# Kernel optimization log

Measured on AMD Instinct MI355X. Metric: run time of the kernel, lower is better.

The kernel has to match this reference:

```python
import jax, jax.numpy as jnp
import numpy as np

N = 50000      # total nodes in batch
E = 640000     # directed edges
G = 64         # graphs in batch
F_IN = 24      # node features
H = 128        # hidden dim
L = 4          # num GCN layers
BN_EPS = 1e-5


def setup_inputs() -> dict:
    key = jax.random.key(0)
    ks = jax.random.split(key, 12)
    s = 0.05  # weight init scale
    return {
        "x": jax.random.normal(ks[0], (N, F_IN), jnp.float32),
        "edge_index": jax.random.randint(ks[1], (2, E), 0, N, dtype=jnp.int32),
        "batch": jnp.sort(jax.random.randint(ks[2], (N,), 0, G, dtype=jnp.int32)),
        "W0": jax.random.normal(ks[3], (F_IN, H), jnp.float32) * s,
        "Wh": jax.random.normal(ks[4], (L - 1, H, H), jnp.float32) * s,
        "b": jnp.zeros((L, H), jnp.float32),
        "bn_gamma": jnp.ones((L, H), jnp.float32),
        "bn_beta": jnp.zeros((L, H), jnp.float32),
        "bn_mean": jax.random.normal(ks[5], (L, H), jnp.float32) * 0.01,
        "bn_var": jnp.ones((L, H), jnp.float32),
        "pool_W": jax.random.normal(ks[6], (2 * H, H), jnp.float32) * s,
        "pool_b": jnp.zeros((H,), jnp.float32),
        "out_W": jax.random.normal(ks[7], (H, H // 2), jnp.float32) * s,
        "out_b": jnp.zeros((H // 2,), jnp.float32),
    }


def reference(x, edge_index, batch, W0, Wh, b, bn_gamma, bn_beta, bn_mean,
              bn_var, pool_W, pool_b, out_W, out_b):
    n = x.shape[0]
    loop = jnp.arange(n, dtype=edge_index.dtype)
    src = jnp.concatenate([edge_index[0], loop])  # [E+N] with self-loops
    dst = jnp.concatenate([edge_index[1], loop])
    # symmetric GCN normalization: deg includes self-loops, so deg >= 1
    deg = jax.ops.segment_sum(jnp.ones_like(dst, x.dtype), dst, num_segments=n)
    dis = jax.lax.rsqrt(deg)
    coef = (dis[src] * dis[dst])[:, None]  # [E+N, 1]

    def gcn_conv(h, W, bias):
        h = h @ W                                   # [N, H]
        msg = h[src] * coef                         # gather + scale
        return jax.ops.segment_sum(msg, dst, num_segments=n) + bias

    Ws = [W0] + [Wh[i] for i in range(Wh.shape[0])]
    h = x
    for i in range(L):
        h = gcn_conv(h, Ws[i], b[i])
        # BatchNorm1d (eval mode) + ReLU; dropout = identity in eval
        h = (h - bn_mean[i]) * jax.lax.rsqrt(bn_var[i] + BN_EPS) * bn_gamma[i] + bn_beta[i]
        h = jax.nn.relu(h)

    counts = jax.ops.segment_sum(jnp.ones((n,), h.dtype), batch, num_segments=G)
    x_mean = jax.ops.segment_sum(h, batch, num_segments=G) / jnp.maximum(counts, 1.0)[:, None]
    x_max = jax.ops.segment_max(h, batch, num_segments=G)
    x_pooled = jnp.concatenate([x_mean, x_max], axis=1)        # [G, 2H]
    x_pooled = jax.nn.relu(x_pooled @ pool_W + pool_b)         # global_pool MLP
    return x_pooled @ out_W + out_b                            # embedding head [G, H//2]
```

## Files before the change

kernel.cpp:

```cpp
#include <hip/hip_runtime.h>
#include <hip/hip_bf16.h>
#include <hip/hip_fp16.h>

#define HD 128
#define BN_EPS 1e-5f
#define PSPLIT 16

typedef __attribute__((ext_vector_type(8))) short short8;
typedef __attribute__((ext_vector_type(4))) float f32x4;

__device__ inline unsigned short f2bf(float v, float& rem) {
    unsigned u = __float_as_uint(v);
    unsigned r = (u + 0x7FFFu + ((u >> 16) & 1u)) >> 16;
    rem = v - __uint_as_float(r << 16);
    return (unsigned short)r;
}

__global__ void k_count(const int* __restrict__ dst, int* __restrict__ counts, int E) {
    int i = blockIdx.x * blockDim.x + threadIdx.x;
    for (; i < E; i += gridDim.x * blockDim.x)
        atomicAdd(&counts[dst[i]], 1);
}

__global__ void k_scan1(const int* __restrict__ counts, int* __restrict__ offs,
                        int* __restrict__ bsums, int n) {
    __shared__ int s[256];
    int t = threadIdx.x, i = blockIdx.x * 256 + t;
    int v = (i < n) ? counts[i] : 0;
    s[t] = v; __syncthreads();
    for (int d = 1; d < 256; d <<= 1) {
        int x = (t >= d) ? s[t - d] : 0;
        __syncthreads(); s[t] += x; __syncthreads();
    }
    if (i < n) offs[i] = s[t] - v;
    if (t == 255) bsums[blockIdx.x] = s[255];
}

__global__ void k_scan2(int* __restrict__ bsums, int nb) {
    __shared__ int s[256];
    int t = threadIdx.x;
    int v = (t < nb) ? bsums[t] : 0;
    s[t] = v; __syncthreads();
    for (int d = 1; d < 256; d <<= 1) {
        int x = (t >= d) ? s[t - d] : 0;
        __syncthreads(); s[t] += x; __syncthreads();
    }
    if (t < nb) bsums[t] = s[t] - v;
}

__global__ void k_scan3(int* __restrict__ offs, const int* __restrict__ bsums,
                        int* __restrict__ cursor, const int* __restrict__ counts,
                        float* __restrict__ dis, int n) {
    int i = blockIdx.x * 256 + threadIdx.x;
    if (i < n) {
        int v = offs[i] + bsums[blockIdx.x];
        offs[i] = v;
        cursor[i] = v;
        dis[i] = rsqrtf((float)(counts[i] + 1));
    }
}

__global__ void k_fill(const int* __restrict__ src, const int* __restrict__ dst,
                       int* __restrict__ cursor, unsigned short* __restrict__ esrc, int E) {
    int i = blockIdx.x * blockDim.x + threadIdx.x;
    for (; i < E; i += gridDim.x * blockDim.x) {
        int s = src[i], d = dst[i];
        int pos = atomicAdd(&cursor[d], 1);
        esrc[pos] = (unsigned short)s;
    }
}

__global__ void k_wsplit(const float* __restrict__ W0, const float* __restrict__ Wh,
                         unsigned short* __restrict__ whi, unsigned short* __restrict__ wlo) {
    int idx = blockIdx.x * 256 + threadIdx.x;
    int l = idx >> 14, rest = idx & 16383;
    int k = rest >> 7, c = rest & 127;
    float val;
    if (l == 0) {
        if (k >= 32) return;
        val = (k < 24) ? W0[k * HD + c] : 0.f;
    } else {
        val = Wh[(size_t)(l - 1) * HD * HD + (size_t)k * HD + c];
    }
    float rem, rem2;
    unsigned short hi = f2bf(val, rem);
    unsigned short lo = f2bf(rem, rem2);
    int cb = c >> 4, kc = k >> 5;
    int lane = (c & 15) | (((k & 31) >> 3) << 4);
    int j = k & 7;
    size_t addr;
    if (l == 0) addr = (size_t)(cb * 64 + lane) * 8 + j;
    else        addr = (size_t)l * 16384 + (size_t)((cb * 4 + kc) * 64 + lane) * 8 + j;
    whi[addr] = hi; wlo[addr] = lo;
}

__global__ void k_agg_x(const float* __restrict__ in, const int* __restrict__ offs,
                        const int* __restrict__ counts, const unsigned short* __restrict__ esrc,
                        const float* __restrict__ dis, unsigned short* __restrict__ ohi,
                        unsigned short* __restrict__ olo, int n) {
    const int FQ = 6, GRP = 8;
    int grp = threadIdx.x / GRP;
    int lane = threadIdx.x % GRP;
    int node = blockIdx.x * (blockDim.x / GRP) + grp;
    if (node >= n) return;
    int rowblk = node >> 4, rr = node & 15;

    if (lane == FQ) {
        size_t base = (size_t)rowblk * 512 + (size_t)(rr + 48) * 8;
        ushort4 z = make_ushort4(0, 0, 0, 0);
        *(ushort4*)(ohi + base) = z; *(ushort4*)(ohi + base + 4) = z;
        *(ushort4*)(olo + base) = z; *(ushort4*)(olo + base + 4) = z;
    }
    if (lane >= FQ) return;

    const float4* in4 = reinterpret_cast<const float4*>(in);
    float dn = dis[node];
    float sl = dn * dn;
    float4 a = in4[(size_t)node * FQ + lane];
    float4 accA = make_float4(sl * a.x, sl * a.y, sl * a.z, sl * a.w);
    float4 accB = make_float4(0.f, 0.f, 0.f, 0.f);

    int e = offs[node], end = e + counts[node];
    for (; e + 3 < end; e += 4) {
        int s0 = esrc[e],     s1 = esrc[e + 1];
        int s2 = esrc[e + 2], s3 = esrc[e + 3];
        float c0 = dis[s0] * dn, c1 = dis[s1] * dn;
        float c2 = dis[s2] * dn, c3 = dis[s3] * dn;
        float4 v0 = in4[(size_t)s0 * FQ + lane];
        float4 v1 = in4[(size_t)s1 * FQ + lane];
        float4 v2 = in4[(size_t)s2 * FQ + lane];
        float4 v3 = in4[(size_t)s3 * FQ + lane];
        accA.x = fmaf(c0, v0.x, fmaf(c2, v2.x, accA.x));
        accA.y = fmaf(c0, v0.y, fmaf(c2, v2.y, accA.y));
        accA.z = fmaf(c0, v0.z, fmaf(c2, v2.z, accA.z));
        accA.w = fmaf(c0, v0.w, fmaf(c2, v2.w, accA.w));
        accB.x = fmaf(c1, v1.x, fmaf(c3, v3.x, accB.x));
        accB.y = fmaf(c1, v1.y, fmaf(c3, v3.y, accB.y));
        accB.z = fmaf(c1, v1.z, fmaf(c3, v3.z, accB.z));
        accB.w = fmaf(c1, v1.w, fmaf(c3, v3.w, accB.w));
    }
    for (; e < end; ++e) {
        int s0 = esrc[e];
        float c0 = dis[s0] * dn;
        float4 v0 = in4[(size_t)s0 * FQ + lane];
        accA.x = fmaf(c0, v0.x, accA.x);
        accA.y = fmaf(c0, v0.y, accA.y);
        accA.z = fmaf(c0, v0.z, accA.z);
        accA.w = fmaf(c0, v0.w, accA.w);
    }
    float4 acc = make_float4(accA.x + accB.x, accA.y + accB.y,
                             accA.z + accB.z, accA.w + accB.w);

    int f0 = lane * 4;
    int lidx = rr | (((f0 & 31) >> 3) << 4);
    int j0 = f0 & 7;
    size_t base = (size_t)rowblk * 512 + (size_t)lidx * 8 + j0;
    float r0, r1, r2, r3, d0;
    ushort4 hi, lo;
    hi.x = f2bf(acc.x, r0); hi.y = f2bf(acc.y, r1);
    hi.z = f2bf(acc.z, r2); hi.w = f2bf(acc.w, r3);
    lo.x = f2bf(r0, d0); lo.y = f2bf(r1, d0);
    lo.z = f2bf(r2, d0); lo.w = f2bf(r3, d0);
    *(ushort4*)(ohi + base) = hi;
    *(ushort4*)(olo + base) = lo;
}

__global__ void k_agg_h(const __half* __restrict__ in, const int* __restrict__ offs,
                        const int* __restrict__ counts, const unsigned short* __restrict__ esrc,
                        const float* __restrict__ dis, unsigned short* __restrict__ ohi,
                        unsigned short* __restrict__ olo, int n) {
    int grp = threadIdx.x >> 5;
    int lane = threadIdx.x & 31;
    int node = blockIdx.x * 8 + grp;
    if (node >= n) return;
    int rowblk = node >> 4, rr = node & 15;

    const float2* in8 = reinterpret_cast<const float2*>(in);
    float dn = dis[node];
    float sl = dn * dn;

    float2 raw = in8[(size_t)node * 32 + lane];
    __half2 p0 = *(__half2*)&raw.x, p1 = *(__half2*)&raw.y;
    float2 f0v = __half22float2(p0), f1v = __half22float2(p1);
    float4 accA = make_float4(sl * f0v.x, sl * f0v.y, sl * f1v.x, sl * f1v.y);
    float4 accB = make_float4(0.f, 0.f, 0.f, 0.f);

    int e = offs[node], end = e + counts[node];
    for (; e + 3 < end; e += 4) {
        int s0 = esrc[e],     s1 = esrc[e + 1];
        int s2 = esrc[e + 2], s3 = esrc[e + 3];
        float c0 = dis[s0] * dn, c1 = dis[s1] * dn;
        float c2 = dis[s2] * dn, c3 = dis[s3] * dn;
        float2 w0 = in8[(size_t)s0 * 32 + lane];
        float2 w1 = in8[(size_t)s1 * 32 + lane];
        float2 w2 = in8[(size_t)s2 * 32 + lane];
        float2 w3 = in8[(size_t)s3 * 32 + lane];
        float2 a0 = __half22float2(*(__half2*)&w0.x), b0 = __half22float2(*(__half2*)&w0.y);
        float2 a1 = __half22float2(*(__half2*)&w1.x), b1 = __half22float2(*(__half2*)&w1.y);
        float2 a2 = __half22float2(*(__half2*)&w2.x), b2 = __half22float2(*(__half2*)&w2.y);
        float2 a3 = __half22float2(*(__half2*)&w3.x), b3 = __half22float2(*(__half2*)&w3.y);
        accA.x = fmaf(c0, a0.x, fmaf(c2, a2.x, accA.x));
        accA.y = fmaf(c0, a0.y, fmaf(c2, a2.y, accA.y));
        accA.z = fmaf(c0, b0.x, fmaf(c2, b2.x, accA.z));
        accA.w = fmaf(c0, b0.y, fmaf(c2, b2.y, accA.w));
        accB.x = fmaf(c1, a1.x, fmaf(c3, a3.x, accB.x));
        accB.y = fmaf(c1, a1.y, fmaf(c3, a3.y, accB.y));
        accB.z = fmaf(c1, b1.x, fmaf(c3, b3.x, accB.z));
        accB.w = fmaf(c1, b1.y, fmaf(c3, b3.y, accB.w));
    }
    for (; e < end; ++e) {
        int s0 = esrc[e];
        float c0 = dis[s0] * dn;
        float2 w0 = in8[(size_t)s0 * 32 + lane];
        float2 a0 = __half22float2(*(__half2*)&w0.x), b0 = __half22float2(*(__half2*)&w0.y);
        accA.x = fmaf(c0, a0.x, accA.x);
        accA.y = fmaf(c0, a0.y, accA.y);
        accA.z = fmaf(c0, b0.x, accA.z);
        accA.w = fmaf(c0, b0.y, accA.w);
    }
    float4 acc = make_float4(accA.x + accB.x, accA.y + accB.y,
                             accA.z + accB.z, accA.w + accB.w);

    int f0 = lane * 4;
    int kc = f0 >> 5;
    int lidx = rr | (((f0 & 31) >> 3) << 4);
    int j0 = f0 & 7;
    size_t base = ((size_t)rowblk * 4 + kc) * 512 + (size_t)lidx * 8 + j0;
    float r0, r1, r2, r3, d0;
    ushort4 hi, lo;
    hi.x = f2bf(acc.x, r0); hi.y = f2bf(acc.y, r1);
    hi.z = f2bf(acc.z, r2); hi.w = f2bf(acc.w, r3);
    lo.x = f2bf(r0, d0); lo.y = f2bf(r1, d0);
    lo.z = f2bf(r2, d0); lo.w = f2bf(r3, d0);
    *(ushort4*)(ohi + base) = hi;
    *(ushort4*)(olo + base) = lo;
}

template<int KC, bool OUT_F16>
__global__ __launch_bounds__(256) void k_gemm_m(
        const unsigned short* __restrict__ agh, const unsigned short* __restrict__ agl,
        const unsigned short* __restrict__ wh, const unsigned short* __restrict__ wl,
        const float* __restrict__ bias, const float* __restrict__ gamma,
        const float* __restrict__ beta, const float* __restrict__ mean,
        const float* __restrict__ var, float* __restrict__ outf,
        __half* __restrict__ outh, int n) {
    __shared__ unsigned short lbh[8 * KC * 512];
    __shared__ unsigned short lbl[8 * KC * 512];
    int tid = threadIdx.x;
    for (int i = tid; i < 1024 * KC; i += 256) {
        ((ushort4*)lbh)[i] = ((const ushort4*)wh)[i];
        ((ushort4*)lbl)[i] = ((const ushort4*)wl)[i];
    }
    __syncthreads();

    int wave = tid >> 6, lane = tid & 63;
    int grb0 = blockIdx.x * 8 + wave * 2;

    f32x4 acc[2][8] = {};

    for (int kc = 0; kc < KC; ++kc) {
        short8 a0h = *(const short8*)(agh + ((size_t)grb0 * KC + kc) * 512 + lane * 8);
        short8 a0l = *(const short8*)(agl + ((size_t)grb0 * KC + kc) * 512 + lane * 8);
        short8 a1h = *(const short8*)(agh + ((size_t)(grb0 + 1) * KC + kc) * 512 + lane * 8);
        short8 a1l = *(const short8*)(agl + ((size_t)(grb0 + 1) * KC + kc) * 512 + lane * 8);
        #pragma unroll
        for (int cb = 0; cb < 8; ++cb) {
            short8 bh = *(const short8*)(lbh + (size_t)((cb * KC + kc) * 64 + lane) * 8);
            short8 bl = *(const short8*)(lbl + (size_t)((cb * KC + kc) * 64 + lane) * 8);
            acc[0][cb] = __builtin_amdgcn_mfma_f32_16x16x32_bf16(a0h, bh, acc[0][cb], 0, 0, 0);
            acc[0][cb] = __builtin_amdgcn_mfma_f32_16x16x32_bf16(a0h, bl, acc[0][cb], 0, 0, 0);
            acc[0][cb] = __builtin_amdgcn_mfma_f32_16x16x32_bf16(a0l, bh, acc[0][cb], 0, 0, 0);
            acc[1][cb] = __builtin_amdgcn_mfma_f32_16x16x32_bf16(a1h, bh, acc[1][cb], 0, 0, 0);
            acc[1][cb] = __builtin_amdgcn_mfma_f32_16x16x32_bf16(a1h, bl, acc[1][cb], 0, 0, 0);
            acc[1][cb] = __builtin_amdgcn_mfma_f32_16x16x32_bf16(a1l, bh, acc[1][cb], 0, 0, 0);
        }
    }

    int colbase = lane & 15;
    float scv[8], shv[8];
    #pragma unroll
    for (int cb = 0; cb < 8; ++cb) {
        int c = cb * 16 + colbase;
        float s = gamma[c] * rsqrtf(var[c] + BN_EPS);
        scv[cb] = s;
        shv[cb] = beta[c] + (bias[c] - mean[c]) * s;
    }
    int r0 = (lane >> 4) * 4;
    #pragma unroll
    for (int rb = 0; rb < 2; ++rb) {
        int rowb = (grb0 + rb) * 16 + r0;
        #pragma unroll
        for (int rg = 0; rg < 4; ++rg) {
            int row = rowb + rg;
            if (row < n) {
                #pragma unroll
                for (int cb = 0; cb < 8; ++cb) {
                    float v = fmaxf(fmaf(acc[rb][cb][rg], scv[cb], shv[cb]), 0.f);
                    if (OUT_F16)
                        outh[(size_t)row * HD + cb * 16 + colbase] = __float2half(v);
                    else
                        outf[(size_t)row * HD + cb * 16 + colbase] = v;
                }
            }
        }
    }
}

__global__ void k_bounds(const int* __restrict__ batch, int* __restrict__ starts,
                         int n, int G) {
    int g = threadIdx.x;
    if (g > G) return;
    int lo = 0, hi = n;
    while (lo < hi) {
        int mid = (lo + hi) >> 1;
        if (batch[mid] < g) lo = mid + 1; else hi = mid;
    }
    starts[g] = lo;
}

__global__ void k_pool(const float* __restrict__ h, const int* __restrict__ starts,
                       float* __restrict__ gsum, unsigned int* __restrict__ gmax) {
    int g = blockIdx.x;
    int slice = blockIdx.y;
    int t = threadIdx.x;
    int s = starts[g], e = starts[g + 1];
    int cnt = e - s;
    int per = (cnt + PSPLIT - 1) / PSPLIT;
    int beg = s + slice * per;
    int end = min(beg + per, e);
    if (beg >= end) return;
    float sum = 0.f, mx = 0.f;
    for (int node = beg; node < end; ++node) {
        float v = h[(size_t)node * HD + t];
        sum += v;
        mx = fmaxf(mx, v);
    }
    atomicAdd(&gsum[g * HD + t], sum);
    atomicMax(&gmax[g * HD + t], __float_as_uint(mx));
}

__global__ void k_mlp1(const float* __restrict__ gsum, const unsigned int* __restrict__ gmax,
                       const int* __restrict__ starts, const float* __restrict__ pool_W,
                       const float* __restrict__ pool_b, float* __restrict__ hid) {
    int g = blockIdx.x, t = threadIdx.x;
    __shared__ float pooled[2 * HD];
    float cntf = fmaxf((float)(starts[g + 1] - starts[g]), 1.f);
    pooled[t] = gsum[g * HD + t] / cntf;
    pooled[HD + t] = __uint_as_float(gmax[g * HD + t]);
    __syncthreads();
    float acc = pool_b[t];
    for (int k = 0; k < 2 * HD; ++k)
        acc += pooled[k] * pool_W[k * HD + t];
    hid[g * HD + t] = fmaxf(acc, 0.f);
}

__global__ void k_mlp2(const float* __restrict__ hid, const float* __restrict__ out_W,
                       const float* __restrict__ out_b, float* __restrict__ out) {
    int g = blockIdx.x, o = threadIdx.x;
    __shared__ float hv[HD];
    hv[o] = hid[g * HD + o];
    hv[o + 64] = hid[g * HD + o + 64];
    __syncthreads();
    float acc = out_b[o];
    for (int j = 0; j < HD; ++j)
        acc += hv[j] * out_W[j * 64 + o];
    out[g * 64 + o] = acc;
}

extern "C" void kernel_launch(void* const* d_in, const int* in_sizes, int n_in,
                              void* d_out, int out_size, void* d_ws, size_t ws_size,
                              hipStream_t stream) {
    const float* x        = (const float*)d_in[0];
    const int*   eidx     = (const int*)d_in[1];
    const int*   batch    = (const int*)d_in[2];
    const float* W0       = (const float*)d_in[3];
    const float* Wh       = (const float*)d_in[4];
    const float* b        = (const float*)d_in[5];
    const float* bn_gamma = (const float*)d_in[6];
    const float* bn_beta  = (const float*)d_in[7];
    const float* bn_mean  = (const float*)d_in[8];
    const float* bn_var   = (const float*)d_in[9];
    const float* pool_W   = (const float*)d_in[10];
    const float* pool_b   = (const float*)d_in[11];
    const float* out_W    = (const float*)d_in[12];
    const float* out_b    = (const float*)d_in[13];
    float* out = (float*)d_out;

    const int N = in_sizes[2];
    const int E = in_sizes[1] / 2;
    const int L = in_sizes[5] / HD;
    const int G = out_size / (HD / 2);

    const int* src = eidx;
    const int* dst = eidx + E;

    const int NBLK = (N + 127) / 128;
    const size_t NRB = (size_t)NBLK * 8;

    char* p = (char*)d_ws;
    float*  h    = (float*)p;  p += (size_t)N * HD * 4;
    __half* hf   = (__half*)p; p += (size_t)NBLK * 128 * HD * 2;
    unsigned short* agh = (unsigned short*)p; p += NRB * 4 * 512 * 2;
    unsigned short* agl = (unsigned short*)p; p += NRB * 4 * 512 * 2;
    unsigned short* whi = (unsigned short*)p; p += (size_t)4 * 16384 * 2;
    unsigned short* wlo = (unsigned short*)p; p += (size_t)4 * 16384 * 2;
    unsigned short* esrc = (unsigned short*)p; p += (((size_t)E * 2 + 15) & ~15ull);
    int*   counts  = (int*)p;   p += (size_t)N * 4;
    float* dis     = (float*)p; p += (size_t)N * 4;
    int*   offs    = (int*)p;   p += (size_t)(N + 1) * 4;
    int*   cursor  = (int*)p;   p += (size_t)N * 4;
    int*   bsums   = (int*)p;   p += 256 * 4;
    float* gsum    = (float*)p; p += (size_t)G * HD * 4;
    unsigned int* gmax = (unsigned int*)p; p += (size_t)G * HD * 4;
    int*   starts  = (int*)p;   p += (size_t)(G + 1) * 4;
    float* hid     = (float*)p; p += (size_t)G * HD * 4;
    (void)ws_size; (void)n_in;

    hipMemsetAsync(counts, 0, (size_t)N * 4, stream);
    hipMemsetAsync(gsum, 0, (size_t)G * HD * 8, stream);

    const int NB = (N + 255) / 256;

    k_count<<<1024, 256, 0, stream>>>(dst, counts, E);
    k_scan1<<<NB, 256, 0, stream>>>(counts, offs, bsums, N);
    k_scan2<<<1, 256, 0, stream>>>(bsums, NB);
    k_scan3<<<NB, 256, 0, stream>>>(offs, bsums, cursor, counts, dis, N);
    k_fill<<<1024, 256, 0, stream>>>(src, dst, cursor, esrc, E);
    k_bounds<<<1, 128, 0, stream>>>(batch, starts, N, G);
    k_wsplit<<<256, 256, 0, stream>>>(W0, Wh, whi, wlo);

    k_agg_x<<<(N + 31) / 32, 256, 0, stream>>>(x, offs, counts, esrc, dis, agh, agl, N);
    k_gemm_m<1, true><<<NBLK, 256, 0, stream>>>(agh, agl, whi, wlo, b, bn_gamma, bn_beta,
                                                bn_mean, bn_var, nullptr, hf, N);

    for (int l = 1; l < L; ++l) {
        k_agg_h<<<(N + 7) / 8, 256, 0, stream>>>(hf, offs, counts, esrc, dis, agh, agl, N);
        if (l < L - 1)
            k_gemm_m<4, true><<<NBLK, 256, 0, stream>>>(agh, agl,
                whi + (size_t)l * 16384, wlo + (size_t)l * 16384,
                b + l * HD, bn_gamma + l * HD, bn_beta + l * HD,
                bn_mean + l * HD, bn_var + l * HD, nullptr, hf, N);
        else
            k_gemm_m<4, false><<<NBLK, 256, 0, stream>>>(agh, agl,
                whi + (size_t)l * 16384, wlo + (size_t)l * 16384,
                b + l * HD, bn_gamma + l * HD, bn_beta + l * HD,
                bn_mean + l * HD, bn_var + l * HD, h, nullptr, N);
    }

    dim3 pgrid(G, PSPLIT);
    k_pool<<<pgrid, HD, 0, stream>>>(h, starts, gsum, gmax);
    k_mlp1<<<G, HD, 0, stream>>>(gsum, gmax, starts, pool_W, pool_b, hid);
    k_mlp2<<<G, 64, 0, stream>>>(hid, out_W, out_b, out);
}
```

Measured before the change: 281.9 us.

## Use single fp16 activations with split fp16 weights for hidden GCN layers

Hidden-layer aggregation now writes one fp16 copy of the aggregated features instead of a bf16 hi/lo pair. The hidden GEMM uses fp16 MFMA with only two products per tile (activation times weight hi and lo) instead of three bf16 products. This halves the aggregation write and GEMM read traffic and cuts MFMA work, at the cost of lower activation precision from fp16 rounding. Separately, the batch-bounds kernel is folded into scan2 and the two head MLP kernels are merged into one, removing launches.

```diff
diff --git a/kernel.cpp b/kernel.cpp
--- a/kernel.cpp
+++ b/kernel.cpp
@@ -7,6 +7,7 @@
 #define PSPLIT 16
 
 typedef __attribute__((ext_vector_type(8))) short short8;
+typedef __attribute__((ext_vector_type(8))) _Float16 half8;
 typedef __attribute__((ext_vector_type(4))) float f32x4;
 
 __device__ inline unsigned short f2bf(float v, float& rem) {
@@ -36,7 +37,9 @@
     if (t == 255) bsums[blockIdx.x] = s[255];
 }
 
-__global__ void k_scan2(int* __restrict__ bsums, int nb) {
+__global__ void k_scan2(int* __restrict__ bsums, int nb,
+                        const int* __restrict__ batch, int* __restrict__ starts,
+                        int n, int G) {
     __shared__ int s[256];
     int t = threadIdx.x;
     int v = (t < nb) ? bsums[t] : 0;
@@ -46,6 +49,14 @@
         __syncthreads(); s[t] += x; __syncthreads();
     }
     if (t < nb) bsums[t] = s[t] - v;
+    if (t <= G) {
+        int lo = 0, hi = n;
+        while (lo < hi) {
+            int mid = (lo + hi) >> 1;
+            if (batch[mid] < t) lo = mid + 1; else hi = mid;
+        }
+        starts[t] = lo;
+    }
 }
 
 __global__ void k_scan3(int* __restrict__ offs, const int* __restrict__ bsums,
@@ -71,27 +82,31 @@
 }
 
 __global__ void k_wsplit(const float* __restrict__ W0, const float* __restrict__ Wh,
-                         unsigned short* __restrict__ whi, unsigned short* __restrict__ wlo) {
+                         unsigned short* __restrict__ whi0, unsigned short* __restrict__ wlo0,
+                         unsigned short* __restrict__ whf, unsigned short* __restrict__ wlf) {
     int idx = blockIdx.x * 256 + threadIdx.x;
     int l = idx >> 14, rest = idx & 16383;
     int k = rest >> 7, c = rest & 127;
-    float val;
-    if (l == 0) {
-        if (k >= 32) return;
-        val = (k < 24) ? W0[k * HD + c] : 0.f;
-    } else {
-        val = Wh[(size_t)(l - 1) * HD * HD + (size_t)k * HD + c];
-    }
-    float rem, rem2;
-    unsigned short hi = f2bf(val, rem);
-    unsigned short lo = f2bf(rem, rem2);
     int cb = c >> 4, kc = k >> 5;
     int lane = (c & 15) | (((k & 31) >> 3) << 4);
     int j = k & 7;
-    size_t addr;
-    if (l == 0) addr = (size_t)(cb * 64 + lane) * 8 + j;
-    else        addr = (size_t)l * 16384 + (size_t)((cb * 4 + kc) * 64 + lane) * 8 + j;
-    whi[addr] = hi; wlo[addr] = lo;
+    if (l == 0) {
+        if (k >= 32) return;
+        float val = (k < 24) ? W0[k * HD + c] : 0.f;
+        float rem, rem2;
+        unsigned short hi = f2bf(val, rem);
+        unsigned short lo = f2bf(rem, rem2);
+        size_t addr = (size_t)(cb * 64 + lane) * 8 + j;
+        whi0[addr] = hi; wlo0[addr] = lo;
+    } else {
+        float val = Wh[(size_t)(l - 1) * HD * HD + (size_t)k * HD + c];
+        __half h = __float2half(val);
+        float rem = val - __half2float(h);
+        __half lo = __float2half(rem);
+        size_t addr = (size_t)(l - 1) * 16384 + (size_t)((cb * 4 + kc) * 64 + lane) * 8 + j;
+        whf[addr] = __half_as_ushort(h);
+        wlf[addr] = __half_as_ushort(lo);
+    }
 }
 
 __global__ void k_agg_x(const float* __restrict__ in, const int* __restrict__ offs,
@@ -167,8 +182,7 @@
 
 __global__ void k_agg_h(const __half* __restrict__ in, const int* __restrict__ offs,
                         const int* __restrict__ counts, const unsigned short* __restrict__ esrc,
-                        const float* __restrict__ dis, unsigned short* __restrict__ ohi,
-                        unsigned short* __restrict__ olo, int n) {
+                        const float* __restrict__ dis, unsigned short* __restrict__ af, int n) {
     int grp = threadIdx.x >> 5;
     int lane = threadIdx.x & 31;
     int node = blockIdx.x * 8 + grp;
@@ -226,28 +240,89 @@
     int lidx = rr | (((f0 & 31) >> 3) << 4);
     int j0 = f0 & 7;
     size_t base = ((size_t)rowblk * 4 + kc) * 512 + (size_t)lidx * 8 + j0;
-    float r0, r1, r2, r3, d0;
-    ushort4 hi, lo;
-    hi.x = f2bf(acc.x, r0); hi.y = f2bf(acc.y, r1);
-    hi.z = f2bf(acc.z, r2); hi.w = f2bf(acc.w, r3);
-    lo.x = f2bf(r0, d0); lo.y = f2bf(r1, d0);
-    lo.z = f2bf(r2, d0); lo.w = f2bf(r3, d0);
-    *(ushort4*)(ohi + base) = hi;
-    *(ushort4*)(olo + base) = lo;
-}
-
-template<int KC, bool OUT_F16>
+    ushort4 hv;
+    hv.x = __half_as_ushort(__float2half(acc.x));
+    hv.y = __half_as_ushort(__float2half(acc.y));
+    hv.z = __half_as_ushort(__float2half(acc.z));
+    hv.w = __half_as_ushort(__float2half(acc.w));
+    *(ushort4*)(af + base) = hv;
+}
+
 __global__ __launch_bounds__(256) void k_gemm_m(
         const unsigned short* __restrict__ agh, const unsigned short* __restrict__ agl,
         const unsigned short* __restrict__ wh, const unsigned short* __restrict__ wl,
         const float* __restrict__ bias, const float* __restrict__ gamma,
         const float* __restrict__ beta, const float* __restrict__ mean,
+        const float* __restrict__ var, __half* __restrict__ outh, int n) {
+    __shared__ unsigned short lbh[8 * 512];
+    __shared__ unsigned short lbl[8 * 512];
+    int tid = threadIdx.x;
+    for (int i = tid; i < 1024; i += 256) {
+        ((ushort4*)lbh)[i] = ((const ushort4*)wh)[i];
+        ((ushort4*)lbl)[i] = ((const ushort4*)wl)[i];
+    }
+    __syncthreads();
+
+    int wave = tid >> 6, lane = tid & 63;
+    int grb0 = blockIdx.x * 8 + wave * 2;
+
+    f32x4 acc[2][8] = {};
+
+    short8 a0h = *(const short8*)(agh + (size_t)grb0 * 512 + lane * 8);
+    short8 a0l = *(const short8*)(agl + (size_t)grb0 * 512 + lane * 8);
+    short8 a1h = *(const short8*)(agh + (size_t)(grb0 + 1) * 512 + lane * 8);
+    short8 a1l = *(const short8*)(agl + (size_t)(grb0 + 1) * 512 + lane * 8);
+    #pragma unroll
+    for (int cb = 0; cb < 8; ++cb) {
+        short8 bh = *(const short8*)(lbh + (size_t)(cb * 64 + lane) * 8);
+        short8 bl = *(const short8*)(lbl + (size_t)(cb * 64 + lane) * 8);
+        acc[0][cb] = __builtin_amdgcn_mfma_f32_16x16x32_bf16(a0h, bh, acc[0][cb], 0, 0, 0);
+        acc[0][cb] = __builtin_amdgcn_mfma_f32_16x16x32_bf16(a0h, bl, acc[0][cb], 0, 0, 0);
+        acc[0][cb] = __builtin_amdgcn_mfma_f32_16x16x32_bf16(a0l, bh, acc[0][cb], 0, 0, 0);
+        acc[1][cb] = __builtin_amdgcn_mfma_f32_16x16x32_bf16(a1h, bh, acc[1][cb], 0, 0, 0);
+        acc[1][cb] = __builtin_amdgcn_mfma_f32_16x16x32_bf16(a1h, bl, acc[1][cb], 0, 0, 0);
+        acc[1][cb] = __builtin_amdgcn_mfma_f32_16x16x32_bf16(a1l, bh, acc[1][cb], 0, 0, 0);
+    }
+
+    int colbase = lane & 15;
+    float scv[8], shv[8];
+    #pragma unroll
+    for (int cb = 0; cb < 8; ++cb) {
+        int c = cb * 16 + colbase;
+        float s = gamma[c] * rsqrtf(var[c] + BN_EPS);
+        scv[cb] = s;
+        shv[cb] = beta[c] + (bias[c] - mean[c]) * s;
+    }
+    int r0 = (lane >> 4) * 4;
+    #pragma unroll
+    for (int rb = 0; rb < 2; ++rb) {
+        int rowb = (grb0 + rb) * 16 + r0;
+        #pragma unroll
+        for (int rg = 0; rg < 4; ++rg) {
+            int row = rowb + rg;
+            if (row < n) {
+                #pragma unroll
+                for (int cb = 0; cb < 8; ++cb) {
+                    float v = fmaxf(fmaf(acc[rb][cb][rg], scv[cb], shv[cb]), 0.f);
+                    outh[(size_t)row * HD + cb * 16 + colbase] = __float2half(v);
+                }
+            }
+        }
+    }
+}
+
+template<bool OUT_F16>
+__global__ __launch_bounds__(256) void k_gemm_h(
+        const unsigned short* __restrict__ af,
+        const unsigned short* __restrict__ wh, const unsigned short* __restrict__ wl,
+        const float* __restrict__ bias, const float* __restrict__ gamma,
+        const float* __restrict__ beta, const float* __restrict__ mean,
         const float* __restrict__ var, float* __restrict__ outf,
         __half* __restrict__ outh, int n) {
-    __shared__ unsigned short lbh[8 * KC * 512];
-    __shared__ unsigned short lbl[8 * KC * 512];
+    __shared__ unsigned short lbh[16384];
+    __shared__ unsigned short lbl[16384];
     int tid = threadIdx.x;
-    for (int i = tid; i < 1024 * KC; i += 256) {
+    for (int i = tid; i < 4096; i += 256) {
         ((ushort4*)lbh)[i] = ((const ushort4*)wh)[i];
         ((ushort4*)lbl)[i] = ((const ushort4*)wl)[i];
     }
@@ -258,21 +333,18 @@
 
     f32x4 acc[2][8] = {};
 
-    for (int kc = 0; kc < KC; ++kc) {
-        short8 a0h = *(const short8*)(agh + ((size_t)grb0 * KC + kc) * 512 + lane * 8);
-        short8 a0l = *(const short8*)(agl + ((size_t)grb0 * KC + kc) * 512 + lane * 8);
-        short8 a1h = *(const short8*)(agh + ((size_t)(grb0 + 1) * KC + kc) * 512 + lane * 8);
-        short8 a1l = *(const short8*)(agl + ((size_t)(grb0 + 1) * KC + kc) * 512 + lane * 8);
+    #pragma unroll
+    for (int kc = 0; kc < 4; ++kc) {
+        half8 a0 = *(const half8*)(af + ((size_t)grb0 * 4 + kc) * 512 + lane * 8);
+        half8 a1 = *(const half8*)(af + ((size_t)(grb0 + 1) * 4 + kc) * 512 + lane * 8);
         #pragma unroll
         for (int cb = 0; cb < 8; ++cb) {
-            short8 bh = *(const short8*)(lbh + (size_t)((cb * KC + kc) * 64 + lane) * 8);
-            short8 bl = *(const short8*)(lbl + (size_t)((cb * KC + kc) * 64 + lane) * 8);
-            acc[0][cb] = __builtin_amdgcn_mfma_f32_16x16x32_bf16(a0h, bh, acc[0][cb], 0, 0, 0);
-            acc[0][cb] = __builtin_amdgcn_mfma_f32_16x16x32_bf16(a0h, bl, acc[0][cb], 0, 0, 0);
-            acc[0][cb] = __builtin_amdgcn_mfma_f32_16x16x32_bf16(a0l, bh, acc[0][cb], 0, 0, 0);
-            acc[1][cb] = __builtin_amdgcn_mfma_f32_16x16x32_bf16(a1h, bh, acc[1][cb], 0, 0, 0);
-            acc[1][cb] = __builtin_amdgcn_mfma_f32_16x16x32_bf16(a1h, bl, acc[1][cb], 0, 0, 0);
-            acc[1][cb] = __builtin_amdgcn_mfma_f32_16x16x32_bf16(a1l, bh, acc[1][cb], 0, 0, 0);
+            half8 bh = *(const half8*)(lbh + (size_t)((cb * 4 + kc) * 64 + lane) * 8);
+            half8 bl = *(const half8*)(lbl + (size_t)((cb * 4 + kc) * 64 + lane) * 8);
+            acc[0][cb] = __builtin_amdgcn_mfma_f32_16x16x32_f16(a0, bh, acc[0][cb], 0, 0, 0);
+            acc[0][cb] = __builtin_amdgcn_mfma_f32_16x16x32_f16(a0, bl, acc[0][cb], 0, 0, 0);
+            acc[1][cb] = __builtin_amdgcn_mfma_f32_16x16x32_f16(a1, bh, acc[1][cb], 0, 0, 0);
+            acc[1][cb] = __builtin_amdgcn_mfma_f32_16x16x32_f16(a1, bl, acc[1][cb], 0, 0, 0);
         }
     }
 
@@ -306,18 +378,6 @@
     }
 }
 
-__global__ void k_bounds(const int* __restrict__ batch, int* __restrict__ starts,
-                         int n, int G) {
-    int g = threadIdx.x;
-    if (g > G) return;
-    int lo = 0, hi = n;
-    while (lo < hi) {
-        int mid = (lo + hi) >> 1;
-        if (batch[mid] < g) lo = mid + 1; else hi = mid;
-    }
-    starts[g] = lo;
-}
-
 __global__ void k_pool(const float* __restrict__ h, const int* __restrict__ starts,
                        float* __restrict__ gsum, unsigned int* __restrict__ gmax) {
     int g = blockIdx.x;
@@ -339,11 +399,13 @@
     atomicMax(&gmax[g * HD + t], __float_as_uint(mx));
 }
 
-__global__ void k_mlp1(const float* __restrict__ gsum, const unsigned int* __restrict__ gmax,
+__global__ void k_head(const float* __restrict__ gsum, const unsigned int* __restrict__ gmax,
                        const int* __restrict__ starts, const float* __restrict__ pool_W,
-                       const float* __restrict__ pool_b, float* __restrict__ hid) {
+                       const float* __restrict__ pool_b, const float* __restrict__ out_W,
+                       const float* __restrict__ out_b, float* __restrict__ out) {
     int g = blockIdx.x, t = threadIdx.x;
     __shared__ float pooled[2 * HD];
+    __shared__ float hid_s[HD];
     float cntf = fmaxf((float)(starts[g + 1] - starts[g]), 1.f);
     pooled[t] = gsum[g * HD + t] / cntf;
     pooled[HD + t] = __uint_as_float(gmax[g * HD + t]);
@@ -351,20 +413,14 @@
     float acc = pool_b[t];
     for (int k = 0; k < 2 * HD; ++k)
         acc += pooled[k] * pool_W[k * HD + t];
-    hid[g * HD + t] = fmaxf(acc, 0.f);
-}
-
-__global__ void k_mlp2(const float* __restrict__ hid, const float* __restrict__ out_W,
-                       const float* __restrict__ out_b, float* __restrict__ out) {
-    int g = blockIdx.x, o = threadIdx.x;
-    __shared__ float hv[HD];
-    hv[o] = hid[g * HD + o];
-    hv[o + 64] = hid[g * HD + o + 64];
+    hid_s[t] = fmaxf(acc, 0.f);
     __syncthreads();
-    float acc = out_b[o];
-    for (int j = 0; j < HD; ++j)
-        acc += hv[j] * out_W[j * 64 + o];
-    out[g * 64 + o] = acc;
+    if (t < 64) {
+        float a2 = out_b[t];
+        for (int j = 0; j < HD; ++j)
+            a2 += hid_s[j] * out_W[j * 64 + t];
+        out[g * 64 + t] = a2;
+    }
 }
 
 extern "C" void kernel_launch(void* const* d_in, const int* in_sizes, int n_in,
@@ -400,10 +456,13 @@
     char* p = (char*)d_ws;
     float*  h    = (float*)p;  p += (size_t)N * HD * 4;
     __half* hf   = (__half*)p; p += (size_t)NBLK * 128 * HD * 2;
-    unsigned short* agh = (unsigned short*)p; p += NRB * 4 * 512 * 2;
-    unsigned short* agl = (unsigned short*)p; p += NRB * 4 * 512 * 2;
-    unsigned short* whi = (unsigned short*)p; p += (size_t)4 * 16384 * 2;
-    unsigned short* wlo = (unsigned short*)p; p += (size_t)4 * 16384 * 2;
+    unsigned short* af  = (unsigned short*)p; p += NRB * 4 * 512 * 2;
+    unsigned short* agh = (unsigned short*)p; p += NRB * 512 * 2;
+    unsigned short* agl = (unsigned short*)p; p += NRB * 512 * 2;
+    unsigned short* whi0 = (unsigned short*)p; p += (size_t)16384 * 2;
+    unsigned short* wlo0 = (unsigned short*)p; p += (size_t)16384 * 2;
+    unsigned short* whf  = (unsigned short*)p; p += (size_t)3 * 16384 * 2;
+    unsigned short* wlf  = (unsigned short*)p; p += (size_t)3 * 16384 * 2;
     unsigned short* esrc = (unsigned short*)p; p += (((size_t)E * 2 + 15) & ~15ull);
     int*   counts  = (int*)p;   p += (size_t)N * 4;
     float* dis     = (float*)p; p += (size_t)N * 4;
@@ -413,7 +472,6 @@
     float* gsum    = (float*)p; p += (size_t)G * HD * 4;
     unsigned int* gmax = (unsigned int*)p; p += (size_t)G * HD * 4;
     int*   starts  = (int*)p;   p += (size_t)(G + 1) * 4;
-    float* hid     = (float*)p; p += (size_t)G * HD * 4;
     (void)ws_size; (void)n_in;
 
     hipMemsetAsync(counts, 0, (size_t)N * 4, stream);
@@ -423,32 +481,30 @@
 
     k_count<<<1024, 256, 0, stream>>>(dst, counts, E);
     k_scan1<<<NB, 256, 0, stream>>>(counts, offs, bsums, N);
-    k_scan2<<<1, 256, 0, stream>>>(bsums, NB);
+    k_scan2<<<1, 256, 0, stream>>>(bsums, NB, batch, starts, N, G);
     k_scan3<<<NB, 256, 0, stream>>>(offs, bsums, cursor, counts, dis, N);
     k_fill<<<1024, 256, 0, stream>>>(src, dst, cursor, esrc, E);
-    k_bounds<<<1, 128, 0, stream>>>(batch, starts, N, G);
-    k_wsplit<<<256, 256, 0, stream>>>(W0, Wh, whi, wlo);
+    k_wsplit<<<256, 256, 0, stream>>>(W0, Wh, whi0, wlo0, whf, wlf);
 
     k_agg_x<<<(N + 31) / 32, 256, 0, stream>>>(x, offs, counts, esrc, dis, agh, agl, N);
-    k_gemm_m<1, true><<<NBLK, 256, 0, stream>>>(agh, agl, whi, wlo, b, bn_gamma, bn_beta,
-                                                bn_mean, bn_var, nullptr, hf, N);
+    k_gemm_m<<<NBLK, 256, 0, stream>>>(agh, agl, whi0, wlo0, b, bn_gamma, bn_beta,
+                                       bn_mean, bn_var, hf, N);
 
     for (int l = 1; l < L; ++l) {
-        k_agg_h<<<(N + 7) / 8, 256, 0, stream>>>(hf, offs, counts, esrc, dis, agh, agl, N);
+        k_agg_h<<<(N + 7) / 8, 256, 0, stream>>>(hf, offs, counts, esrc, dis, af, N);
+        const unsigned short* wh_l = whf + (size_t)(l - 1) * 16384;
+        const unsigned short* wl_l = wlf + (size_t)(l - 1) * 16384;
         if (l < L - 1)
-            k_gemm_m<4, true><<<NBLK, 256, 0, stream>>>(agh, agl,
-                whi + (size_t)l * 16384, wlo + (size_t)l * 16384,
+            k_gemm_h<true><<<NBLK, 256, 0, stream>>>(af, wh_l, wl_l,
                 b + l * HD, bn_gamma + l * HD, bn_beta + l * HD,
                 bn_mean + l * HD, bn_var + l * HD, nullptr, hf, N);
         else
-            k_gemm_m<4, false><<<NBLK, 256, 0, stream>>>(agh, agl,
-                whi + (size_t)l * 16384, wlo + (size_t)l * 16384,
+            k_gemm_h<false><<<NBLK, 256, 0, stream>>>(af, wh_l, wl_l,
                 b + l * HD, bn_gamma + l * HD, bn_beta + l * HD,
                 bn_mean + l * HD, bn_var + l * HD, h, nullptr, N);
     }
 
     dim3 pgrid(G, PSPLIT);
     k_pool<<<pgrid, HD, 0, stream>>>(h, starts, gsum, gmax);
-    k_mlp1<<<G, HD, 0, stream>>>(gsum, gmax, starts, pool_W, pool_b, hid);
-    k_mlp2<<<G, 64, 0, stream>>>(hid, out_W, out_b, out);
-}
+    k_head<<<G, HD, 0, stream>>>(gsum, gmax, starts, pool_W, pool_b, out_W, out_b, out);
+}
```

Result: no change. 279.8 us (-0.8%).
